# Performance work log

Measured on AMD Instinct MI355X. Metric: run time of the kernel, lower is better.

The kernel has to match this reference:

```python
import jax, jax.numpy as jnp
import numpy as np
from jax import lax

TOP_K = 2

def _unfold(x_img, k):
    # F.unfold(kernel=k, stride=k): [B,C,H,W] -> [B, C*k*k, L], column index c*k*k + kh*k + kw
    B, C, H, W = x_img.shape
    Hp, Wp = H // k, W // k
    u = x_img.reshape(B, C, Hp, k, Wp, k).transpose(0, 1, 3, 5, 2, 4)
    return u.reshape(B, C * k * k, Hp * Wp)

def _fold(p, k, H, W):
    # F.fold inverse of non-overlapping unfold: [B, C*k*k, L] -> [B,C,H,W]
    B = p.shape[0]
    C = p.shape[1] // (k * k)
    Hp, Wp = H // k, W // k
    u = p.reshape(B, C, k, k, Hp, Wp).transpose(0, 1, 4, 2, 5, 3)
    return u.reshape(B, C, H, W)

def setup_inputs() -> dict:
    key = jax.random.key(0)
    ks = jax.random.split(key, 6)
    B, H, W, C, F, E, P = 8, 64, 64, 384, 1536, 8, 4
    N = H * W
    x = jax.random.normal(ks[0], (B, N, C), dtype=jnp.float32)
    gate_w = jax.random.normal(ks[1], (E, C, P, P), dtype=jnp.float32) * 0.01
    w1 = jax.random.normal(ks[2], (E, C, F), dtype=jnp.float32) * (1.0 / np.sqrt(C))
    b1 = jax.random.normal(ks[3], (E, F), dtype=jnp.float32) * 0.01
    w2 = jax.random.normal(ks[4], (E, F, C), dtype=jnp.float32) * (1.0 / np.sqrt(F))
    b2 = jax.random.normal(ks[5], (E, C), dtype=jnp.float32) * 0.01
    return {"x": x, "gate_w": gate_w, "w1": w1, "b1": b1, "w2": w2, "b2": b2, "H": H, "W": W}

def reference(x, gate_w, w1, b1, w2, b2, H, W):
    B, N, C = x.shape
    E, _, P, _ = gate_w.shape
    k2 = P * P
    Hp, Wp = H // P, W // P
    L = Hp * Wp
    x_img = jnp.transpose(x, (0, 2, 1)).reshape(B, C, H, W)
    # router: strided conv -> logits per patch
    logits_map = lax.conv_general_dilated(
        x_img, gate_w, window_strides=(P, P), padding='VALID',
        dimension_numbers=('NCHW', 'OIHW', 'NCHW'))  # [B,E,Hp,Wp]
    router_logits = jnp.transpose(logits_map, (0, 2, 3, 1)).reshape(B, L, E)
    probs = jax.nn.softmax(router_logits, axis=-1)
    ew, ei = lax.top_k(probs, TOP_K)  # [B,L,topk]
    ew = ew / (jnp.sum(ew, axis=-1, keepdims=True) + 1e-9)
    # expand to token level (faithful to original's reshape/flatten ordering)
    ei_tok = jnp.broadcast_to(ei[:, :, None, :], (B, L, k2, TOP_K)).reshape(-1, TOP_K)
    ew_tok = jnp.broadcast_to(ew[:, :, None, :], (B, L, k2, TOP_K)).reshape(-1, TOP_K)
    # unfold + the original's (scrambled) reshape(B, C, L, k2)
    U = _unfold(x_img, P)  # [B, C*k2, L]
    x_patches = jnp.transpose(U.reshape(B, C, L, k2), (0, 2, 3, 1))  # [B,L,k2,C]
    flat_x = x_patches.reshape(-1, C)  # [T,C], T = B*L*k2
    # combine weights: zero for experts not in top-k == masked dispatch math
    cw = jnp.zeros((flat_x.shape[0], E), dtype=flat_x.dtype)
    for kk in range(TOP_K):
        cw = cw + jax.nn.one_hot(ei_tok[:, kk], E, dtype=flat_x.dtype) * ew_tok[:, kk:kk + 1]
    out = jnp.zeros_like(flat_x)
    for e in range(E):
        h = jax.nn.gelu(flat_x @ w1[e] + b1[e], approximate=False)
        y = h @ w2[e] + b2[e]
        out = out + cw[:, e:e + 1] * y
    # fold back (mirrors original's reshape/permute exactly)
    o = jnp.transpose(out.reshape(B, L, k2, C), (0, 3, 1, 2)).reshape(B, C * k2, L)
    out_img = _fold(o, P, H, W)  # [B,C,H,W]
    # original: output.transpose(1,2).reshape(B,N,C) on NCHW tensor
    output = jnp.transpose(out_img, (0, 2, 1, 3)).reshape(B, N, C)
    return output
```

## Files before the change

kernel.cpp:

```cpp
#include <hip/hip_runtime.h>
#include <hip/hip_bf16.h>

#define BB   8
#define HH   64
#define WWID 64
#define CC   384
#define FF   1536
#define EE   8
#define LL   256
#define MTOTMAX 66560
#define NTMAX   520

typedef unsigned short ushort_t;
typedef __attribute__((ext_vector_type(4))) unsigned short u16x4;
typedef __attribute__((ext_vector_type(8))) short          s16x8;
typedef __attribute__((ext_vector_type(4))) float          f32x4;

__device__ __forceinline__ float bf2f(ushort_t u) {
  union { unsigned int i; float f; } v; v.i = ((unsigned int)u) << 16; return v.f;
}
__device__ __forceinline__ ushort_t f2bf(float f) {
  union { float f; unsigned int i; } v; v.f = f;
  unsigned int u = v.i;
  u += 0x7fffu + ((u >> 16) & 1u);
  return (ushort_t)(u >> 16);
}
__device__ __forceinline__ float gelu_f(float x) {
  float u  = 0.70710678118654752f * x;
  float au = fabsf(u);
  float t  = 1.0f / (1.0f + 0.3275911f * au);
  float poly = t * (0.254829592f + t * (-0.284496736f + t * (1.421413741f +
               t * (-1.453152027f + t * 1.061405429f))));
  float ea = 1.0f - poly * __expf(-au * au);
  float erfv = (x < 0.f) ? -ea : ea;
  return 0.5f * x * (1.0f + erfv);
}

#define GLDS(g, l) __builtin_amdgcn_global_load_lds( \
    (const __attribute__((address_space(1))) void*)(g), \
    (__attribute__((address_space(3))) void*)(l), 16, 0, 0)

__global__ __launch_bounds__(256) void k_transpose(const float* __restrict__ src,
                                                   ushort_t* __restrict__ dst,
                                                   int R, int Cd) {
  __shared__ ushort_t tile[32][33];
  int e  = blockIdx.z;
  int c0 = blockIdx.x * 32, r0 = blockIdx.y * 32;
  int tx = threadIdx.x & 31, ty = threadIdx.x >> 5;
  const float* s = src + (size_t)e * R * Cd;
  ushort_t*    d = dst + (size_t)e * R * Cd;
  #pragma unroll
  for (int i = 0; i < 32; i += 8)
    tile[ty + i][tx] = f2bf(s[(size_t)(r0 + ty + i) * Cd + c0 + tx]);
  __syncthreads();
  #pragma unroll
  for (int i = 0; i < 32; i += 8)
    d[(size_t)(c0 + ty + i) * R + r0 + tx] = tile[tx][ty + i];
}

__global__ void k_tgw(const float* __restrict__ gw, float* __restrict__ gwt) {
  int e = blockIdx.x, t = threadIdx.x;
  for (int i = t; i < CC * 16; i += 256) {
    int c = i >> 4, p = i & 15;
    gwt[((size_t)e * 16 + p) * CC + c] = gw[(size_t)e * CC * 16 + i];
  }
}

__global__ __launch_bounds__(256) void k_router(const float* __restrict__ x,
                                                const float* __restrict__ gwt,
                                                int* __restrict__ re, float* __restrict__ rw,
                                                int* __restrict__ cnt) {
  int bid = blockIdx.x;
  int b = bid >> 8, l2 = bid & 255;
  int hp = l2 >> 4, wp = l2 & 15;
  int t = threadIdx.x;
  int e = t >> 5, lane = t & 31;
  const float* xb = x + (size_t)b * (HH * WWID) * CC;
  const float* ge = gwt + (size_t)e * 16 * CC;
  float acc = 0.f;
  #pragma unroll
  for (int p = 0; p < 16; ++p) {
    int pix = (hp * 4 + (p >> 2)) * 64 + wp * 4 + (p & 3);
    const float* xr = xb + (size_t)pix * CC;
    const float* gr = ge + (size_t)p * CC;
    #pragma unroll
    for (int it = 0; it < 3; ++it) {
      f32x4 xv = *reinterpret_cast<const f32x4*>(xr + it * 128 + lane * 4);
      f32x4 gv = *reinterpret_cast<const f32x4*>(gr + it * 128 + lane * 4);
      acc += xv.x * gv.x + xv.y * gv.y + xv.z * gv.z + xv.w * gv.w;
    }
  }
  #pragma unroll
  for (int d = 16; d; d >>= 1) acc += __shfl_down(acc, d, 32);
  __shared__ float logits[EE];
  if (lane == 0) logits[e] = acc;
  __syncthreads();
  if (t == 0) {
    float m = logits[0];
    #pragma unroll
    for (int i = 1; i < EE; ++i) m = fmaxf(m, logits[i]);
    float p[EE]; float s = 0.f;
    #pragma unroll
    for (int i = 0; i < EE; ++i) { p[i] = __expf(logits[i] - m); s += p[i]; }
    #pragma unroll
    for (int i = 0; i < EE; ++i) p[i] /= s;
    int e0 = 0;
    #pragma unroll
    for (int i = 1; i < EE; ++i) if (p[i] > p[e0]) e0 = i;
    int e1 = (e0 == 0) ? 1 : 0;
    #pragma unroll
    for (int i = 0; i < EE; ++i) if (i != e0 && p[i] > p[e1]) e1 = i;
    float s2 = p[e0] + p[e1] + 1e-9f;
    re[bid * 2 + 0] = e0;  re[bid * 2 + 1] = e1;
    rw[bid * 2 + 0] = p[e0] / s2;  rw[bid * 2 + 1] = p[e1] / s2;
    atomicAdd(&cnt[e0], 16);
    atomicAdd(&cnt[e1], 16);
  }
}

__global__ void k_pad(const int* __restrict__ cnt, int* __restrict__ cntp,
                      int* __restrict__ basep, int* __restrict__ tile2e,
                      int* __restrict__ gids, float* __restrict__ gwts) {
  __shared__ int s_cnt[EE], s_cntp[EE], s_base[EE + 1];
  int t = threadIdx.x;
  if (t == 0) {
    int b = 0;
    for (int e = 0; e < EE; ++e) {
      int c  = cnt[e];
      int cp = (c + 127) & ~127;
      s_cnt[e] = c; s_cntp[e] = cp; s_base[e] = b;
      b += cp;
    }
    s_base[EE] = b;
  }
  __syncthreads();
  if (t < EE) { cntp[t] = s_cntp[t]; basep[t] = s_base[t]; }
  if (t == EE) basep[EE] = s_base[EE];
  int ntot = s_base[EE] >> 7;
  for (int g = t; g < ntot; g += 256) {
    int e = 0;
    #pragma unroll
    for (int i = 1; i < EE; ++i) if (g * 128 >= s_base[i]) e = i;
    tile2e[g] = e;
  }
  for (int e = 0; e < EE; ++e)
    for (int i = s_cnt[e] + t; i < s_cntp[e]; i += 256) {
      gids[s_base[e] + i] = -1;
      gwts[s_base[e] + i] = 0.f;
    }
}

__global__ void k_assign(const int* __restrict__ re, const float* __restrict__ rw,
                         const int* __restrict__ basep, int* __restrict__ cnt2,
                         int* __restrict__ gids, float* __restrict__ gwts,
                         int* __restrict__ inv) {
  int i = blockIdx.x * blockDim.x + threadIdx.x;
  if (i >= BB * LL * 2) return;
  int pat = i >> 1, slot = i & 1;
  int b = pat >> 8, l2 = pat & 255;
  int e = re[i];
  float w = rw[i];
  int t2 = l2 >> 4, hp = l2 & 15;
  int kh = t2 >> 2, kw = t2 & 3;
  int h = hp * 4 + kh;
  int row = basep[e] + atomicAdd(&cnt2[e], 16);
  #pragma unroll
  for (int j = 0; j < 16; ++j) {
    int wpix = j * 4 + kw;
    int pix = (b << 12) + (h << 6) + wpix;
    gids[row + j] = pix;
    gwts[row + j] = w;
    inv[(slot << 15) + pix] = row + j;
  }
}

__global__ __launch_bounds__(256) void k_gather(const float* __restrict__ x,
                                                const int* __restrict__ gids,
                                                const int* __restrict__ basep,
                                                ushort_t* __restrict__ Xc, int t0) {
  int g = t0 + blockIdx.x;
  if (g * 128 >= basep[EE]) return;
  __shared__ int s_id[128];
  int t = threadIdx.x;
  if (t < 128) s_id[t] = gids[g * 128 + t];
  __syncthreads();
  ushort_t* dst = Xc + (size_t)blockIdx.x * 128 * CC;
  for (int i = t; i < 128 * 96; i += 256) {
    int row = i / 96, ch = (i % 96) * 4;
    int id = s_id[row];
    f32x4 v = (f32x4){0.f, 0.f, 0.f, 0.f};
    if (id >= 0) v = *reinterpret_cast<const f32x4*>(x + (size_t)(id & 32767) * CC + ch);
    u16x4 o = {f2bf(v.x), f2bf(v.y), f2bf(v.z), f2bf(v.w)};
    *reinterpret_cast<u16x4*>(dst + (size_t)row * CC + ch) = o;
  }
}

#define GSTEP(RD, ST, KNEXT, DOST)                                            \
  {                                                                           \
    if (DOST) {                                                               \
      _Pragma("unroll")                                                       \
      for (int c = 0; c < 4; ++c)                                             \
        GLDS(src_c[c] + (KNEXT), (ST) + (w * 4 + c) * 512);                   \
    }                                                                         \
    s16x8 af[4], bf[4];                                                       \
    _Pragma("unroll")                                                         \
    for (int i = 0; i < 4; ++i)                                               \
      af[i] = *reinterpret_cast<const s16x8*>((RD) + ((w & 1) * 4 + i) * 512 + lane * 8); \
    _Pragma("unroll")                                                         \
    for (int j = 0; j < 4; ++j)                                               \
      bf[j] = *reinterpret_cast<const s16x8*>((RD) + (8 + (w >> 1) * 4 + j) * 512 + lane * 8); \
    __builtin_amdgcn_s_setprio(1);                                            \
    _Pragma("unroll")                                                         \
    for (int i = 0; i < 4; ++i)                                               \
      _Pragma("unroll")                                                       \
      for (int j = 0; j < 4; ++j)                                             \
        acc[i][j] = __builtin_amdgcn_mfma_f32_16x16x32_bf16(af[i], bf[j], acc[i][j], 0, 0, 0); \
    __builtin_amdgcn_s_setprio(0);                                            \
    __syncthreads();                                                          \
  }

template<int K, int NOUT, bool GELU, bool OUTG>
__global__ __launch_bounds__(256, 4) void k_gemm(const ushort_t* __restrict__ A,
                                                 const ushort_t* __restrict__ Bsrc,
                                                 const float* __restrict__ bias,
                                                 const int* __restrict__ basep,
                                                 const int* __restrict__ tile2e,
                                                 const float* __restrict__ gwts,
                                                 ushort_t* __restrict__ out, int t0) {
  int g = t0 + blockIdx.y;
  if (g * 128 >= basep[EE]) return;
  int e = tile2e[g], ng = blockIdx.x;
  __shared__ ushort_t S[2][16 * 512];
  __shared__ float s_w[128];
  int t = threadIdx.x, w = t >> 6, lane = t & 63;
  int l15 = lane & 15, q = lane >> 4;
  if (!GELU && t < 128) s_w[t] = gwts[g * 128 + t];
  const ushort_t* a_src = A + ((size_t)e * NOUT + ng * 128) * K;
  const ushort_t* b_src = Bsrc + (size_t)blockIdx.y * 128 * K;

  const ushort_t* src_c[4];
  #pragma unroll
  for (int c = 0; c < 4; ++c) {
    int ch = w * 4 + c;
    src_c[c] = (ch < 8)
      ? a_src + (size_t)(ch * 16 + l15) * K + q * 8
      : b_src + (size_t)((ch - 8) * 16 + l15) * K + q * 8;
  }

  f32x4 acc[4][4];
  #pragma unroll
  for (int i = 0; i < 4; ++i)
    #pragma unroll
    for (int j = 0; j < 4; ++j) acc[i][j] = (f32x4){0.f, 0.f, 0.f, 0.f};

  ushort_t* S0 = &S[0][0];
  ushort_t* S1 = &S[1][0];

  #pragma unroll
  for (int c = 0; c < 4; ++c) GLDS(src_c[c], S0 + (w * 4 + c) * 512);
  __syncthreads();

  constexpr int NIT = K / 32;
  for (int it = 0; it < NIT; it += 2) {
    GSTEP(S0, S1, (size_t)(it + 1) * 32, true);
    GSTEP(S1, S0, (size_t)(it + 2) * 32, it + 2 < NIT);
  }

  int nb = ng * 128 + (w & 1) * 64 + q * 4;
  f32x4 bv[4];
  #pragma unroll
  for (int i = 0; i < 4; ++i)
    bv[i] = *reinterpret_cast<const f32x4*>(bias + (size_t)e * NOUT + nb + i * 16);
  ushort_t* ob = out + (OUTG ? (size_t)g : (size_t)blockIdx.y) * 128 * NOUT;
  #pragma unroll
  for (int j = 0; j < 4; ++j) {
    int m = (w >> 1) * 64 + j * 16 + l15;
    float wt = GELU ? 1.f : s_w[m];
    ushort_t* op = ob + (size_t)m * NOUT + nb;
    #pragma unroll
    for (int i = 0; i < 4; ++i) {
      u16x4 v;
      #pragma unroll
      for (int r = 0; r < 4; ++r) {
        float xv = acc[i][j][r] + bv[i][r];
        v[r] = f2bf(GELU ? gelu_f(xv) : xv * wt);
      }
      *reinterpret_cast<u16x4*>(op + i * 16) = v;
    }
  }
}

__global__ __launch_bounds__(256) void k_final(const ushort_t* __restrict__ y,
                                               const int* __restrict__ inv,
                                               float* __restrict__ out) {
  int bid = blockIdx.x;
  __shared__ float tile[64][193];
  __shared__ int s_r0[64], s_r1[64];
  int t = threadIdx.x;
  if (t < 64) {
    s_r0[t] = inv[(bid << 6) + t];
    s_r1[t] = inv[32768 + (bid << 6) + t];
  }
  __syncthreads();
  float* dst = out + (size_t)bid * CC * WWID;
  #pragma unroll
  for (int half = 0; half < 2; ++half) {
    int c0 = half * 192;
    for (int i = t; i < 64 * 48; i += 256) {
      int w = i / 48, c4 = (i % 48) * 4;
      u16x4 a = *reinterpret_cast<const u16x4*>(y + (size_t)s_r0[w] * CC + c0 + c4);
      u16x4 b = *reinterpret_cast<const u16x4*>(y + (size_t)s_r1[w] * CC + c0 + c4);
      #pragma unroll
      for (int k = 0; k < 4; ++k)
        tile[w][c4 + k] = bf2f(a[k]) + bf2f(b[k]);
    }
    __syncthreads();
    for (int i = t; i < 64 * 192; i += 256) {
      int cl = i / 64, w = i % 64;
      dst[(size_t)(c0 + cl) * WWID + w] = tile[w][cl];
    }
    __syncthreads();
  }
}

extern "C" void kernel_launch(void* const* d_in, const int* in_sizes, int n_in,
                              void* d_out, int out_size, void* d_ws, size_t ws_size,
                              hipStream_t stream) {
  const float* x  = (const float*)d_in[0];
  const float* gw = (const float*)d_in[1];
  const float* w1 = (const float*)d_in[2];
  const float* b1 = (const float*)d_in[3];
  const float* w2 = (const float*)d_in[4];
  const float* b2 = (const float*)d_in[5];

  const size_t fixed = (size_t)EE * FF * CC * 2 * 2
                     + (size_t)MTOTMAX * CC * 2
                     + (size_t)EE * 16 * CC * 4
                     + (size_t)MTOTMAX * 4 * 2
                     + (size_t)65536 * 4
                     + (size_t)BB * LL * 2 * 4 * 2
                     + (size_t)NTMAX * 4
                     + 1024;
  const int cands[6] = {32768, 16384, 8192, 4096, 2048, 1024};
  int MC = 1024;
  for (int i = 0; i < 6; ++i)
    if (fixed + (size_t)cands[i] * 3840 <= ws_size) { MC = cands[i]; break; }
  const int npass = (MTOTMAX + MC - 1) / MC;
  const int ntile = MC / 128;

  char* ws = (char*)d_ws;
  size_t off = 0;
  ushort_t* Xc   = (ushort_t*)(ws + off); off += (size_t)MC * CC * 2;
  ushort_t* Hc   = (ushort_t*)(ws + off); off += (size_t)MC * FF * 2;
  ushort_t* w1t  = (ushort_t*)(ws + off); off += (size_t)EE * FF * CC * 2;
  ushort_t* w2t  = (ushort_t*)(ws + off); off += (size_t)EE * FF * CC * 2;
  ushort_t* y    = (ushort_t*)(ws + off); off += (size_t)MTOTMAX * CC * 2;
  float* gwt   = (float*)(ws + off); off += (size_t)EE * 16 * CC * 4;
  int*   gids  = (int*)(ws + off);   off += (size_t)MTOTMAX * 4;
  float* gwts  = (float*)(ws + off); off += (size_t)MTOTMAX * 4;
  int*   inv   = (int*)(ws + off);   off += (size_t)65536 * 4;
  int*   re    = (int*)(ws + off);   off += (size_t)BB * LL * 2 * 4;
  float* rw    = (float*)(ws + off); off += (size_t)BB * LL * 2 * 4;
  int*   tile2e= (int*)(ws + off);   off += (size_t)NTMAX * 4;
  int*   cnt   = (int*)(ws + off);   off += 64;
  int*   cnt2  = (int*)(ws + off);   off += 64;
  int*   cntp  = (int*)(ws + off);   off += 64;
  int*   basep = (int*)(ws + off);   off += 64;

  hipMemsetAsync(cnt, 0, 128, stream);

  k_transpose<<<dim3(FF / 32, CC / 32, EE), 256, 0, stream>>>(w1, w1t, CC, FF);
  k_transpose<<<dim3(CC / 32, FF / 32, EE), 256, 0, stream>>>(w2, w2t, FF, CC);
  k_tgw<<<EE, 256, 0, stream>>>(gw, gwt);
  k_router<<<BB * LL, 256, 0, stream>>>(x, gwt, re, rw, cnt);
  k_pad<<<1, 256, 0, stream>>>(cnt, cntp, basep, tile2e, gids, gwts);
  k_assign<<<16, 256, 0, stream>>>(re, rw, basep, cnt2, gids, gwts, inv);

  for (int p = 0; p < npass; ++p) {
    int t0 = p * ntile;
    k_gather<<<ntile, 256, 0, stream>>>(x, gids, basep, Xc, t0);
    k_gemm<CC, FF, true,  false><<<dim3(FF / 128, ntile), 256, 0, stream>>>(
        w1t, Xc, b1, basep, tile2e, (const float*)nullptr, Hc, t0);
    k_gemm<FF, CC, false, true ><<<dim3(CC / 128, ntile), 256, 0, stream>>>(
        w2t, Hc, b2, basep, tile2e, gwts, y, t0);
  }
  k_final<<<BB * HH, 256, 0, stream>>>(y, inv, (float*)d_out);
}
```

Before: 696.3 us.

## Restructure GEMM k-loop to prefetch two stages ahead and use sigmoid-form GELU

```diff
diff --git a/kernel.cpp b/kernel.cpp
--- a/kernel.cpp
+++ b/kernel.cpp
@@ -26,14 +26,11 @@
   return (ushort_t)(u >> 16);
 }
 __device__ __forceinline__ float gelu_f(float x) {
-  float u  = 0.70710678118654752f * x;
-  float au = fabsf(u);
-  float t  = 1.0f / (1.0f + 0.3275911f * au);
-  float poly = t * (0.254829592f + t * (-0.284496736f + t * (1.421413741f +
-               t * (-1.453152027f + t * 1.061405429f))));
-  float ea = 1.0f - poly * __expf(-au * au);
-  float erfv = (x < 0.f) ? -ea : ea;
-  return 0.5f * x * (1.0f + erfv);
+  float x2 = x * x;
+  float t  = __builtin_fmaf(x2, -0.10294325f, -2.3022082f);
+  float e  = __builtin_amdgcn_exp2f(x * t);
+  float r  = __builtin_amdgcn_rcpf(1.0f + e);
+  return x * r;
 }
 
 #define GLDS(g, l) __builtin_amdgcn_global_load_lds( \
@@ -195,13 +192,17 @@
   }
 }
 
-#define GSTEP(RD, ST, KNEXT, DOST)                                            \
+#define STAGE(DST, KOFF)                                                      \
+  { _Pragma("unroll")                                                         \
+    for (int c = 0; c < 4; ++c)                                               \
+      GLDS(src_c[c] + (KOFF), (DST) + (w * 4 + c) * 512); }
+
+#define PHASE(VM, RD, DOST, STDST, KOFF)                                      \
   {                                                                           \
-    if (DOST) {                                                               \
-      _Pragma("unroll")                                                       \
-      for (int c = 0; c < 4; ++c)                                             \
-        GLDS(src_c[c] + (KNEXT), (ST) + (w * 4 + c) * 512);                   \
-    }                                                                         \
+    asm volatile("s_waitcnt vmcnt(" VM ")" ::: "memory");                     \
+    __builtin_amdgcn_s_barrier();                                             \
+    asm volatile("" ::: "memory");                                            \
+    __builtin_amdgcn_sched_barrier(0);                                        \
     s16x8 af[4], bf[4];                                                       \
     _Pragma("unroll")                                                         \
     for (int i = 0; i < 4; ++i)                                               \
@@ -209,6 +210,11 @@
     _Pragma("unroll")                                                         \
     for (int j = 0; j < 4; ++j)                                               \
       bf[j] = *reinterpret_cast<const s16x8*>((RD) + (8 + (w >> 1) * 4 + j) * 512 + lane * 8); \
+    asm volatile("s_waitcnt lgkmcnt(0)" ::: "memory");                        \
+    __builtin_amdgcn_sched_barrier(0);                                        \
+    __builtin_amdgcn_s_barrier();                                             \
+    asm volatile("" ::: "memory");                                            \
+    if (DOST) STAGE(STDST, KOFF);                                             \
     __builtin_amdgcn_s_setprio(1);                                            \
     _Pragma("unroll")                                                         \
     for (int i = 0; i < 4; ++i)                                               \
@@ -216,7 +222,6 @@
       for (int j = 0; j < 4; ++j)                                             \
         acc[i][j] = __builtin_amdgcn_mfma_f32_16x16x32_bf16(af[i], bf[j], acc[i][j], 0, 0, 0); \
     __builtin_amdgcn_s_setprio(0);                                            \
-    __syncthreads();                                                          \
   }
 
 template<int K, int NOUT, bool GELU, bool OUTG>
@@ -231,10 +236,8 @@
   if (g * 128 >= basep[EE]) return;
   int e = tile2e[g], ng = blockIdx.x;
   __shared__ ushort_t S[2][16 * 512];
-  __shared__ float s_w[128];
   int t = threadIdx.x, w = t >> 6, lane = t & 63;
   int l15 = lane & 15, q = lane >> 4;
-  if (!GELU && t < 128) s_w[t] = gwts[g * 128 + t];
   const ushort_t* a_src = A + ((size_t)e * NOUT + ng * 128) * K;
   const ushort_t* b_src = Bsrc + (size_t)blockIdx.y * 128 * K;
 
@@ -253,18 +256,19 @@
     #pragma unroll
     for (int j = 0; j < 4; ++j) acc[i][j] = (f32x4){0.f, 0.f, 0.f, 0.f};
 
-  ushort_t* S0 = &S[0][0];
-  ushort_t* S1 = &S[1][0];
-
-  #pragma unroll
-  for (int c = 0; c < 4; ++c) GLDS(src_c[c], S0 + (w * 4 + c) * 512);
-  __syncthreads();
+  ushort_t* S0v = &S[0][0];
+  ushort_t* S1v = &S[1][0];
+
+  STAGE(S0v, 0);
+  STAGE(S1v, 32);
 
   constexpr int NIT = K / 32;
-  for (int it = 0; it < NIT; it += 2) {
-    GSTEP(S0, S1, (size_t)(it + 1) * 32, true);
-    GSTEP(S1, S0, (size_t)(it + 2) * 32, it + 2 < NIT);
-  }
+  for (int it = 0; it < NIT - 2; it += 2) {
+    PHASE("4", S0v, true, S0v, (size_t)(it + 2) * 32);
+    PHASE("4", S1v, true, S1v, (size_t)(it + 3) * 32);
+  }
+  PHASE("4", S0v, false, S0v, 0);
+  PHASE("0", S1v, false, S1v, 0);
 
   int nb = ng * 128 + (w & 1) * 64 + q * 4;
   f32x4 bv[4];
@@ -275,7 +279,7 @@
   #pragma unroll
   for (int j = 0; j < 4; ++j) {
     int m = (w >> 1) * 64 + j * 16 + l15;
-    float wt = GELU ? 1.f : s_w[m];
+    float wt = GELU ? 1.f : gwts[g * 128 + m];
     ushort_t* op = ob + (size_t)m * NOUT + nb;
     #pragma unroll
     for (int i = 0; i < 4; ++i) {
```

Result: faster. 678.1 us (-2.6%).
